# Kernel tuning notes

Hardware: AMD Instinct MI355X
Metric: run time of the kernel (lower is better)

The kernel has to match this reference:

```python
import jax, jax.numpy as jnp
import numpy as np

DIM = 1024
HEADS = 16
DIM_HEAD = 64
DIM_INNER = HEADS * DIM_HEAD
R_MAJOR = 2.0
R_MINOR = 1.0
EPS = 1e-10
ATTN_SCALE = DIM_HEAD ** 0.5  # torch SDPA `scale` is a multiplier on q@k^T
S_QK_FACTOR = float(DIM)      # Scale forward multiplier: init / scale = 1.0 / (1/dim)


def toroidal_norm(t, axis=-1, R=R_MAJOR, r=R_MINOR, eps=EPS):
    """Project onto sphere, scale first half of `axis` by R, second by r, renormalize."""
    axis = axis % t.ndim
    n = jnp.linalg.norm(t, axis=axis, keepdims=True)
    sp = t / jnp.clip(n, eps)
    d = t.shape[axis]
    h = d // 2
    scale = jnp.concatenate([jnp.full((h,), R, t.dtype), jnp.full((d - h,), r, t.dtype)])
    bshape = [1] * t.ndim
    bshape[axis] = d
    tp = sp * scale.reshape(bshape)
    n2 = jnp.linalg.norm(tp, axis=axis, keepdims=True)
    return tp / jnp.clip(n2, eps)


def setup_inputs() -> dict:
    key = jax.random.key(0)
    ks = jax.random.split(key, 5)
    b, n = 4, 1024
    x = jax.random.normal(ks[0], (b, n, DIM), jnp.float32)
    std = DIM ** -0.5
    w_q = jax.random.normal(ks[1], (DIM_INNER, DIM), jnp.float32) * std
    w_k = jax.random.normal(ks[2], (DIM_INNER, DIM), jnp.float32) * std
    w_v = jax.random.normal(ks[3], (DIM_INNER, DIM), jnp.float32) * std
    w_o = jax.random.normal(ks[4], (DIM, DIM_INNER), jnp.float32) * std
    qk_scale_param = jnp.full((DIM_INNER,), 1.0 / DIM, jnp.float32)  # Scale init
    return {"x": x, "w_q": w_q, "w_k": w_k, "w_v": w_v, "w_o": w_o,
            "qk_scale_param": qk_scale_param}


def reference(x, w_q, w_k, w_v, w_o, qk_scale_param):
    b, n, _ = x.shape
    # parametrized (toroidal-normed) projection weights
    wq = toroidal_norm(w_q, axis=-1)
    wk = toroidal_norm(w_k, axis=-1)
    wv = toroidal_norm(w_v, axis=-1)
    wo = toroidal_norm(w_o, axis=0)  # norm_dim_in=False -> dim=0

    q = jnp.einsum('bnd,ed->bne', x, wq).reshape(b, n, HEADS, DIM_HEAD).transpose(0, 2, 1, 3)
    k = jnp.einsum('bnd,ed->bne', x, wk).reshape(b, n, HEADS, DIM_HEAD).transpose(0, 2, 1, 3)
    v = jnp.einsum('bnd,ed->bne', x, wv).reshape(b, n, HEADS, DIM_HEAD).transpose(0, 2, 1, 3)

    # toroidal norm over head dim
    q = toroidal_norm(q, axis=-1)
    k = toroidal_norm(k, axis=-1)

    # learned per-channel qk scale: param * (init / scale)
    s = (qk_scale_param * S_QK_FACTOR).reshape(HEADS, 1, DIM_HEAD)
    q = q * s

    scores = jnp.einsum('bhnd,bhmd->bhnm', q, k) * ATTN_SCALE
    causal = jnp.tril(jnp.ones((n, n), bool))
    scores = jnp.where(causal, scores, jnp.finfo(scores.dtype).min)
    attn = jax.nn.softmax(scores, axis=-1)
    out = jnp.einsum('bhnm,bhmd->bhnd', attn, v)  # b h n d

    out = out.transpose(0, 2, 1, 3).reshape(b, n, DIM_INNER)
    return jnp.einsum('bne,de->bnd', out, wo)
```

## Files before the change

### kernel.cpp

```cpp
#include <hip/hip_runtime.h>
#include <hip/hip_bf16.h>

#define HEADS 16
#define DH    64
#define BATCH 4
#define SEQ   1024
#define DIMD  1024
#define TOK   4096

typedef __attribute__((ext_vector_type(8))) short bf16x8;
typedef __attribute__((ext_vector_type(4))) float f32x4;
typedef __attribute__((ext_vector_type(16))) float f32x16;

typedef const void __attribute__((address_space(1)))* gas1_t;
typedef void __attribute__((address_space(3)))* las3_t;

#define GLOAD16(g,l) __builtin_amdgcn_global_load_lds((gas1_t)(g),(las3_t)(l),16,0,0)
#define MFMA_BF16(a,b,c) __builtin_amdgcn_mfma_f32_16x16x32_bf16((a),(b),(c),0,0,0)
#define MFMA32(a,b,c) __builtin_amdgcn_mfma_f32_32x32x16_bf16((a),(b),(c),0,0,0)
#define ZERO16 {0.f,0.f,0.f,0.f,0.f,0.f,0.f,0.f,0.f,0.f,0.f,0.f,0.f,0.f,0.f,0.f}

__device__ __forceinline__ ushort f2bf(float f){
  __hip_bfloat16 h = __float2bfloat16(f);
  return *reinterpret_cast<ushort*>(&h);
}
__device__ __forceinline__ uint packbf2(float a, float b){
  return (uint)f2bf(a) | ((uint)f2bf(b) << 16);
}
__device__ __forceinline__ uint xswap32(uint x){
  return (uint)__shfl_xor((int)x, 32);
}

__global__ __launch_bounds__(256) void cast_x_kernel(const float* __restrict__ x,
                                                     ushort* __restrict__ xb){
  int i = blockIdx.x*256 + threadIdx.x;
  const float4* x4 = (const float4*)x;
  float4 a = x4[2*i], b = x4[2*i+1];
  union { ushort s[8]; uint4 u; } uu;
  uu.s[0]=f2bf(a.x); uu.s[1]=f2bf(a.y); uu.s[2]=f2bf(a.z); uu.s[3]=f2bf(a.w);
  uu.s[4]=f2bf(b.x); uu.s[5]=f2bf(b.y); uu.s[6]=f2bf(b.z); uu.s[7]=f2bf(b.w);
  ((uint4*)xb)[i] = uu.u;
}

__global__ __launch_bounds__(256) void norm_rows_kernel(
    const float* __restrict__ wq, const float* __restrict__ wk, const float* __restrict__ wv,
    ushort* __restrict__ oq, ushort* __restrict__ ok, ushort* __restrict__ ov){
  int row = blockIdx.x & 1023;
  int m = blockIdx.x >> 10;
  const float* src = (m==0)?wq:((m==1)?wk:wv);
  ushort* dst = (m==0)?oq:((m==1)?ok:ov);
  int t = threadIdx.x;
  float4 v = ((const float4*)(src + (size_t)row*1024))[t];
  float sc = (t<128)?2.f:1.f;
  float ss = sc*sc*(v.x*v.x + v.y*v.y + v.z*v.z + v.w*v.w);
  #pragma unroll
  for (int off=1; off<64; off<<=1) ss += __shfl_xor(ss, off);
  __shared__ float part[4];
  int w = t>>6, lane = t&63;
  if (lane==0) part[w]=ss;
  __syncthreads();
  float tot = part[0]+part[1]+part[2]+part[3];
  float inv = rsqrtf(fmaxf(tot,1e-20f)) * sc;
  union { ushort s[4]; uint2 u; } o;
  o.s[0]=f2bf(v.x*inv); o.s[1]=f2bf(v.y*inv); o.s[2]=f2bf(v.z*inv); o.s[3]=f2bf(v.w*inv);
  ((uint2*)(dst + (size_t)row*1024))[t] = o.u;
}

__global__ __launch_bounds__(256) void cast_wo_kernel(const float* __restrict__ wo,
                                                      ushort* __restrict__ wob){
  int i = blockIdx.x*256 + threadIdx.x;
  float sc = ((i>>7) < 512) ? 2.f : 1.f;
  const float4* x4 = (const float4*)wo;
  float4 a = x4[2*i], b = x4[2*i+1];
  union { ushort s[8]; uint4 u; } uu;
  uu.s[0]=f2bf(a.x*sc); uu.s[1]=f2bf(a.y*sc); uu.s[2]=f2bf(a.z*sc); uu.s[3]=f2bf(a.w*sc);
  uu.s[4]=f2bf(b.x*sc); uu.s[5]=f2bf(b.y*sc); uu.s[6]=f2bf(b.z*sc); uu.s[7]=f2bf(b.w*sc);
  ((uint4*)wob)[i] = uu.u;
}

__global__ __launch_bounds__(256) void wo_part_kernel(const float* __restrict__ wo,
                                                      float* __restrict__ part){
  int rb = blockIdx.x, t = threadIdx.x;
  float4 a = {0.f,0.f,0.f,0.f};
  #pragma unroll 4
  for (int r=0;r<32;r++){
    int row = rb*32+r;
    float4 v = ((const float4*)wo)[row*256 + t];
    float s2 = (row<512)?4.f:1.f;
    a.x += s2*v.x*v.x; a.y += s2*v.y*v.y; a.z += s2*v.z*v.z; a.w += s2*v.w*v.w;
  }
  ((float4*)part)[rb*256 + t] = a;
}
__global__ __launch_bounds__(256) void wo_csum_kernel(const float* __restrict__ part,
                                                      float* __restrict__ colsum){
  int c = blockIdx.x*256 + threadIdx.x;
  float s = 0.f;
  #pragma unroll
  for (int j=0;j<32;j++) s += part[j*1024 + c];
  colsum[c] = s;
}

template<int NZ>
__global__ __launch_bounds__(256, 2) void gemm_fused_kernel(
    const ushort* __restrict__ A,
    const ushort* __restrict__ B0, const ushort* __restrict__ B1, const ushort* __restrict__ B2,
    void* dst0, void* dst1, void* dst2,
    const float* __restrict__ qparam, const float* __restrict__ colsum, int K)
{
  __shared__ ushort As[64*32];
  __shared__ ushort Bs[NZ*128*32];
  const int bm = blockIdx.x*64, bn = blockIdx.y*128;
  const int tid = threadIdx.x, lane = tid&63, w = tid>>6;
  const int wr = w>>1, wc = w&1;
  const int l15 = lane&15, l4 = lane>>4;
  const int srow = lane>>2, sch = lane&3;

  const f32x4 zero4 = {0.f,0.f,0.f,0.f};
  f32x4 acc[NZ][2][4];
  #pragma unroll
  for (int z=0;z<NZ;z++)
    #pragma unroll
    for (int m=0;m<2;m++)
      #pragma unroll
      for (int n=0;n<4;n++) acc[z][m][n] = zero4;

  for (int k0=0; k0<K; k0+=32){
    __syncthreads();
    GLOAD16(A + (size_t)(bm + w*16 + srow)*K + k0 + sch*8, &As[w*512]);
    #pragma unroll
    for (int j=0;j<NZ*2;j++){
      int seg = j*4 + w;
      int z = seg>>3, s = seg&7;
      const ushort* Bp = (z==0)?B0:((z==1)?B1:B2);
      GLOAD16(Bp + (size_t)(bn + s*16 + srow)*K + k0 + sch*8, &Bs[seg*512]);
    }
    __syncthreads();
    bf16x8 af[2];
    #pragma unroll
    for (int m=0;m<2;m++)
      af[m] = *(const bf16x8*)&As[(wr*32 + m*16 + l15)*32 + l4*8];
    #pragma unroll
    for (int z=0;z<NZ;z++){
      bf16x8 bfr[4];
      #pragma unroll
      for (int n=0;n<4;n++)
        bfr[n] = *(const bf16x8*)&Bs[z*4096 + (wc*64 + n*16 + l15)*32 + l4*8];
      #pragma unroll
      for (int m=0;m<2;m++)
        #pragma unroll
        for (int n=0;n<4;n++)
          acc[z][m][n] = MFMA_BF16(af[m], bfr[n], acc[z][m][n]);
    }
  }

  if (NZ==3){
    #pragma unroll
    for (int z=0;z<3;z++){
      ushort* dst = (ushort*)((z==0)?dst0:((z==1)?dst1:dst2));
      float qs[4];
      #pragma unroll
      for (int n=0;n<4;n++){
        int e = bn + wc*64 + n*16 + l15;
        if (z==0)      qs[n] = qparam[e]*8192.f*1.44269504088896f;
        else if (z==2) qs[n] = rsqrtf(fmaxf(colsum[e],1e-20f));
        else           qs[n] = 1.f;
      }
      #pragma unroll
      for (int m=0;m<2;m++){
        float ssq[4] = {0.f,0.f,0.f,0.f};
        if (z<2){
          #pragma unroll
          for (int reg=0;reg<4;reg++){
            float s=0.f;
            #pragma unroll
            for (int n=0;n<4;n++){
              float scl2 = (n<2)?4.f:1.f;
              float vv = acc[z][m][n][reg];
              s += scl2*vv*vv;
            }
            ssq[reg]=s;
          }
          #pragma unroll
          for (int d=1; d<16; d<<=1){
            #pragma unroll
            for (int reg=0;reg<4;reg++) ssq[reg] += __shfl_xor(ssq[reg], d);
          }
        }
        #pragma unroll
        for (int n=0;n<4;n++){
          float scl = (n<2)?2.f:1.f;
          #pragma unroll
          for (int reg=0;reg<4;reg++){
            float val = acc[z][m][n][reg];
            if (z<2) val = val*scl*rsqrtf(fmaxf(ssq[reg],1e-20f))*qs[n];
            else     val = val*qs[n];
            int row = bm + wr*32 + m*16 + l4*4 + reg;
            int col = bn + wc*64 + n*16 + l15;
            int b = row>>10, nn = row&1023, h = col>>6, d = col&63;
            if (z==2)
              dst[(((size_t)b*HEADS+h)*DH + d)*SEQ + nn] = f2bf(val);
            else
              dst[(((size_t)b*HEADS+h)*SEQ + nn)*DH + d] = f2bf(val);
          }
        }
      }
    }
  } else {
    float* outp = (float*)dst0;
    #pragma unroll
    for (int m=0;m<2;m++)
      #pragma unroll
      for (int n=0;n<4;n++)
        #pragma unroll
        for (int reg=0;reg<4;reg++){
          int row = bm + wr*32 + m*16 + l4*4 + reg;
          int col = bn + wc*64 + n*16 + l15;
          outp[(size_t)row*DIMD + col] = acc[0][m][n][reg];
        }
  }
}

template<int NS, bool MASK>
__device__ __forceinline__ void attn_iter(
    const ushort* __restrict__ Kp, const ushort* __restrict__ Vp,
    int kvb, const bf16x8 (&qf)[4], int l31, int l1,
    f32x16& o0, f32x16& o1, float& m_s, float& l_s)
{
  bf16x8 kfa[4], kfb[4];
  #pragma unroll
  for (int md=0; md<4; md++)
    kfa[md] = *(const bf16x8*)&Kp[(size_t)(kvb + l31)*DH + md*16 + l1*8];
  if (NS==2){
    #pragma unroll
    for (int md=0; md<4; md++)
      kfb[md] = *(const bf16x8*)&Kp[(size_t)(kvb + 32 + l31)*DH + md*16 + l1*8];
  }
  bf16x8 vf0[2*NS], vf1[2*NS];
  #pragma unroll
  for (int kc=0; kc<2*NS; kc++){
    vf0[kc] = *(const bf16x8*)&Vp[(size_t)l31*SEQ      + kvb + kc*16 + l1*8];
    vf1[kc] = *(const bf16x8*)&Vp[(size_t)(32+l31)*SEQ + kvb + kc*16 + l1*8];
  }

  f32x16 s0 = ZERO16, s1 = ZERO16;
  __builtin_amdgcn_s_setprio(1);
  #pragma unroll
  for (int md=0; md<4; md++) s0 = MFMA32(kfa[md], qf[md], s0);
  if (NS==2){
    #pragma unroll
    for (int md=0; md<4; md++) s1 = MFMA32(kfb[md], qf[md], s1);
  }
  __builtin_amdgcn_s_setprio(0);

  if (MASK){
    f32x16& sm = (NS==2) ? s1 : s0;
    #pragma unroll
    for (int r=0;r<16;r++){
      int kvl = (r&3) + 8*(r>>2) + 4*l1;
      if (kvl > l31) sm[r] = -3.0e38f;
    }
  }

  float mx = -3.0e38f;
  #pragma unroll
  for (int r=0;r<16;r++) mx = fmaxf(mx, s0[r]);
  if (NS==2){
    #pragma unroll
    for (int r=0;r<16;r++) mx = fmaxf(mx, s1[r]);
  }
  mx = fmaxf(mx, __shfl_xor(mx, 32));
  float mnew = fmaxf(m_s, mx);
  float alpha = __builtin_amdgcn_exp2f(m_s - mnew);
  m_s = mnew;
  float rs = 0.f;
  #pragma unroll
  for (int r=0;r<16;r++){ s0[r] = __builtin_amdgcn_exp2f(s0[r]-mnew); rs += s0[r]; }
  if (NS==2){
    #pragma unroll
    for (int r=0;r<16;r++){ s1[r] = __builtin_amdgcn_exp2f(s1[r]-mnew); rs += s1[r]; }
  }
  rs += __shfl_xor(rs, 32);
  l_s = l_s*alpha + rs;

  #pragma unroll
  for (int r=0;r<16;r++){ o0[r] *= alpha; o1[r] *= alpha; }

  uint ru[16];
  #pragma unroll
  for (int j=0;j<8;j++) ru[j] = packbf2(s0[2*j], s0[2*j+1]);
  if (NS==2){
    #pragma unroll
    for (int j=0;j<8;j++) ru[8+j] = packbf2(s1[2*j], s1[2*j+1]);
  }
  union U4 { uint u[4]; bf16x8 v; };
  U4 fr[2*NS];
  #pragma unroll
  for (int j=0;j<NS;j++){
    uint px[8];
    #pragma unroll
    for (int k=0;k<8;k++) px[k] = xswap32(ru[8*j+k]);
    fr[2*j].u[0]   = l1 ? px[2]      : ru[8*j+0];
    fr[2*j].u[1]   = l1 ? px[3]      : ru[8*j+1];
    fr[2*j].u[2]   = l1 ? ru[8*j+2]  : px[0];
    fr[2*j].u[3]   = l1 ? ru[8*j+3]  : px[1];
    fr[2*j+1].u[0] = l1 ? px[6]      : ru[8*j+4];
    fr[2*j+1].u[1] = l1 ? px[7]      : ru[8*j+5];
    fr[2*j+1].u[2] = l1 ? ru[8*j+6]  : px[4];
    fr[2*j+1].u[3] = l1 ? ru[8*j+7]  : px[5];
  }

  __builtin_amdgcn_s_setprio(1);
  #pragma unroll
  for (int kc=0; kc<2*NS; kc++){
    o0 = MFMA32(vf0[kc], fr[kc].v, o0);
    o1 = MFMA32(vf1[kc], fr[kc].v, o1);
  }
  __builtin_amdgcn_s_setprio(0);
}

__device__ __forceinline__ void process_tile(
    int t, int par, int bh,
    const ushort* __restrict__ Q, const ushort* __restrict__ K,
    const ushort* __restrict__ VT, ushort* __restrict__ O,
    int l31, int l1)
{
  const size_t base  = (size_t)bh * SEQ * DH;
  const size_t vbase = (size_t)bh * DH * SEQ;
  const ushort* Kp = K + base;
  const ushort* Vp = VT + vbase;
  const int qbase = t*64 + par*32;

  bf16x8 qf[4];
  #pragma unroll
  for (int md=0; md<4; md++)
    qf[md] = *(const bf16x8*)&Q[base + (size_t)(qbase + l31)*DH + md*16 + l1*8];

  f32x16 o0 = ZERO16, o1 = ZERO16;
  float m_s = -3.0e38f, l_s = 0.f;

  for (int kt=0; kt<t; kt++)
    attn_iter<2,false>(Kp, Vp, kt*64, qf, l31, l1, o0, o1, m_s, l_s);
  if (par) attn_iter<2,true>(Kp, Vp, t*64, qf, l31, l1, o0, o1, m_s, l_s);
  else     attn_iter<1,true>(Kp, Vp, t*64, qf, l31, l1, o0, o1, m_s, l_s);

  float li = 1.0f / l_s;
  int b = bh >> 4, hh = bh & 15;
  int n = qbase + l31;
  ushort* orow = O + ((size_t)b*SEQ + n)*DIMD + hh*64;
  #pragma unroll
  for (int r=0;r<16;r++){
    int dl = (r&3) + 8*(r>>2) + 4*l1;
    orow[dl]    = f2bf(o0[r]*li);
    orow[32+dl] = f2bf(o1[r]*li);
  }
}

__global__ __launch_bounds__(256, 2) void attn_kernel(
    const ushort* __restrict__ Q, const ushort* __restrict__ K, const ushort* __restrict__ VT,
    ushort* __restrict__ O)
{
  int id = blockIdx.x;
  int p  = id >> 6;
  int r  = id & 63;
  int bh = (r&7)*8 + (r>>3);
  int tid = threadIdx.x, wi = tid>>6, lane = tid&63;
  int l31 = lane & 31, l1 = lane >> 5;
  int sel = (wi & 1) ^ (bh & 1);
  int t   = sel ? (15-p) : p;
  int par = wi >> 1;
  process_tile(t, par, bh, Q, K, VT, O, l31, l1);
}

extern "C" void kernel_launch(void* const* d_in, const int* in_sizes, int n_in,
                              void* d_out, int out_size, void* d_ws, size_t ws_size,
                              hipStream_t stream)
{
  const float* x      = (const float*)d_in[0];
  const float* w_q    = (const float*)d_in[1];
  const float* w_k    = (const float*)d_in[2];
  const float* w_v    = (const float*)d_in[3];
  const float* w_o    = (const float*)d_in[4];
  const float* qparam = (const float*)d_in[5];
  char* ws = (char*)d_ws;
  const size_t MB = 1u<<20;
  ushort* xb  = (ushort*)(ws);
  ushort* wqb = (ushort*)(ws + 8*MB);
  ushort* wkb = (ushort*)(ws + 10*MB);
  ushort* wvb = (ushort*)(ws + 12*MB);
  ushort* wob = (ushort*)(ws + 14*MB);
  ushort* qd  = (ushort*)(ws + 16*MB);
  ushort* kd  = (ushort*)(ws + 24*MB);
  ushort* vd  = (ushort*)(ws + 32*MB);
  ushort* att = xb;
  float* part = (float*)(ws + 16*MB);
  float* colsum = (float*)d_out + (out_size - 1024);

  cast_x_kernel<<<dim3(2048), dim3(256), 0, stream>>>(x, xb);
  norm_rows_kernel<<<dim3(3072), dim3(256), 0, stream>>>(w_q, w_k, w_v, wqb, wkb, wvb);
  cast_wo_kernel<<<dim3(512), dim3(256), 0, stream>>>(w_o, wob);
  wo_part_kernel<<<dim3(32), dim3(256), 0, stream>>>(w_o, part);
  wo_csum_kernel<<<dim3(4), dim3(256), 0, stream>>>(part, colsum);
  gemm_fused_kernel<3><<<dim3(64,8), dim3(256), 0, stream>>>(
      xb, wqb, wkb, wvb, (void*)qd, (void*)kd, (void*)vd, qparam, colsum, DIMD);
  attn_kernel<<<dim3(512), dim3(256), 0, stream>>>(qd, kd, vd, att);
  gemm_fused_kernel<1><<<dim3(64,8), dim3(256), 0, stream>>>(
      att, wob, wob, wob, d_out, nullptr, nullptr, nullptr, nullptr, DIMD);
}
```

Measured before the change: 126.3 us.

## Merge preprocessing kernels into one launch and change GEMM LDS tile layout

Combines the x cast, q/k/v weight row normalisation, w_o cast and w_o column-partial-sum kernels into a single prep kernel that branches on block index. This removes three launches and the gaps between them. The partial-sum buffer moves to its own workspace region so it cannot collide with q data. The GEMM global-to-LDS load mapping also changes: each lane now loads row lane&15 and chunk lane>>4, and the fragment reads use a matching chunk-major LDS layout. The aim is to change LDS bank access patterns for the MFMA operand reads.

Measured after the change: 143.5 us. 1.14x slower.

```diff
diff --git a/kernel.cpp b/kernel.cpp
--- a/kernel.cpp
+++ b/kernel.cpp
@@ -31,66 +31,66 @@
   return (uint)__shfl_xor((int)x, 32);
 }
 
-__global__ __launch_bounds__(256) void cast_x_kernel(const float* __restrict__ x,
-                                                     ushort* __restrict__ xb){
-  int i = blockIdx.x*256 + threadIdx.x;
-  const float4* x4 = (const float4*)x;
-  float4 a = x4[2*i], b = x4[2*i+1];
-  union { ushort s[8]; uint4 u; } uu;
-  uu.s[0]=f2bf(a.x); uu.s[1]=f2bf(a.y); uu.s[2]=f2bf(a.z); uu.s[3]=f2bf(a.w);
-  uu.s[4]=f2bf(b.x); uu.s[5]=f2bf(b.y); uu.s[6]=f2bf(b.z); uu.s[7]=f2bf(b.w);
-  ((uint4*)xb)[i] = uu.u;
-}
-
-__global__ __launch_bounds__(256) void norm_rows_kernel(
+__global__ __launch_bounds__(256) void prep_kernel(
+    const float* __restrict__ x,
     const float* __restrict__ wq, const float* __restrict__ wk, const float* __restrict__ wv,
-    ushort* __restrict__ oq, ushort* __restrict__ ok, ushort* __restrict__ ov){
-  int row = blockIdx.x & 1023;
-  int m = blockIdx.x >> 10;
-  const float* src = (m==0)?wq:((m==1)?wk:wv);
-  ushort* dst = (m==0)?oq:((m==1)?ok:ov);
-  int t = threadIdx.x;
-  float4 v = ((const float4*)(src + (size_t)row*1024))[t];
-  float sc = (t<128)?2.f:1.f;
-  float ss = sc*sc*(v.x*v.x + v.y*v.y + v.z*v.z + v.w*v.w);
-  #pragma unroll
-  for (int off=1; off<64; off<<=1) ss += __shfl_xor(ss, off);
-  __shared__ float part[4];
-  int w = t>>6, lane = t&63;
-  if (lane==0) part[w]=ss;
-  __syncthreads();
-  float tot = part[0]+part[1]+part[2]+part[3];
-  float inv = rsqrtf(fmaxf(tot,1e-20f)) * sc;
-  union { ushort s[4]; uint2 u; } o;
-  o.s[0]=f2bf(v.x*inv); o.s[1]=f2bf(v.y*inv); o.s[2]=f2bf(v.z*inv); o.s[3]=f2bf(v.w*inv);
-  ((uint2*)(dst + (size_t)row*1024))[t] = o.u;
-}
-
-__global__ __launch_bounds__(256) void cast_wo_kernel(const float* __restrict__ wo,
-                                                      ushort* __restrict__ wob){
-  int i = blockIdx.x*256 + threadIdx.x;
-  float sc = ((i>>7) < 512) ? 2.f : 1.f;
-  const float4* x4 = (const float4*)wo;
-  float4 a = x4[2*i], b = x4[2*i+1];
-  union { ushort s[8]; uint4 u; } uu;
-  uu.s[0]=f2bf(a.x*sc); uu.s[1]=f2bf(a.y*sc); uu.s[2]=f2bf(a.z*sc); uu.s[3]=f2bf(a.w*sc);
-  uu.s[4]=f2bf(b.x*sc); uu.s[5]=f2bf(b.y*sc); uu.s[6]=f2bf(b.z*sc); uu.s[7]=f2bf(b.w*sc);
-  ((uint4*)wob)[i] = uu.u;
-}
-
-__global__ __launch_bounds__(256) void wo_part_kernel(const float* __restrict__ wo,
-                                                      float* __restrict__ part){
-  int rb = blockIdx.x, t = threadIdx.x;
-  float4 a = {0.f,0.f,0.f,0.f};
-  #pragma unroll 4
-  for (int r=0;r<32;r++){
-    int row = rb*32+r;
-    float4 v = ((const float4*)wo)[row*256 + t];
-    float s2 = (row<512)?4.f:1.f;
-    a.x += s2*v.x*v.x; a.y += s2*v.y*v.y; a.z += s2*v.z*v.z; a.w += s2*v.w*v.w;
-  }
-  ((float4*)part)[rb*256 + t] = a;
-}
+    const float* __restrict__ wo,
+    ushort* __restrict__ xb,
+    ushort* __restrict__ oq, ushort* __restrict__ ok, ushort* __restrict__ ov,
+    ushort* __restrict__ wob, float* __restrict__ part)
+{
+  __shared__ float sp[4];
+  int bid = blockIdx.x, t = threadIdx.x;
+  if (bid < 2048){
+    int i = bid*256 + t;
+    const float4* x4 = (const float4*)x;
+    float4 a = x4[2*i], b = x4[2*i+1];
+    union { ushort s[8]; uint4 u; } uu;
+    uu.s[0]=f2bf(a.x); uu.s[1]=f2bf(a.y); uu.s[2]=f2bf(a.z); uu.s[3]=f2bf(a.w);
+    uu.s[4]=f2bf(b.x); uu.s[5]=f2bf(b.y); uu.s[6]=f2bf(b.z); uu.s[7]=f2bf(b.w);
+    ((uint4*)xb)[i] = uu.u;
+  } else if (bid < 5120){
+    int bb = bid - 2048;
+    int row = bb & 1023;
+    int m = bb >> 10;
+    const float* src = (m==0)?wq:((m==1)?wk:wv);
+    ushort* dst = (m==0)?oq:((m==1)?ok:ov);
+    float4 v = ((const float4*)(src + (size_t)row*1024))[t];
+    float sc = (t<128)?2.f:1.f;
+    float ss = sc*sc*(v.x*v.x + v.y*v.y + v.z*v.z + v.w*v.w);
+    #pragma unroll
+    for (int off=1; off<64; off<<=1) ss += __shfl_xor(ss, off);
+    int w = t>>6, lane = t&63;
+    if (lane==0) sp[w]=ss;
+    __syncthreads();
+    float tot = sp[0]+sp[1]+sp[2]+sp[3];
+    float inv = rsqrtf(fmaxf(tot,1e-20f)) * sc;
+    union { ushort s[4]; uint2 u; } o;
+    o.s[0]=f2bf(v.x*inv); o.s[1]=f2bf(v.y*inv); o.s[2]=f2bf(v.z*inv); o.s[3]=f2bf(v.w*inv);
+    ((uint2*)(dst + (size_t)row*1024))[t] = o.u;
+  } else if (bid < 5632){
+    int i = (bid-5120)*256 + t;
+    float sc = ((i>>7) < 512) ? 2.f : 1.f;
+    const float4* x4 = (const float4*)wo;
+    float4 a = x4[2*i], b = x4[2*i+1];
+    union { ushort s[8]; uint4 u; } uu;
+    uu.s[0]=f2bf(a.x*sc); uu.s[1]=f2bf(a.y*sc); uu.s[2]=f2bf(a.z*sc); uu.s[3]=f2bf(a.w*sc);
+    uu.s[4]=f2bf(b.x*sc); uu.s[5]=f2bf(b.y*sc); uu.s[6]=f2bf(b.z*sc); uu.s[7]=f2bf(b.w*sc);
+    ((uint4*)wob)[i] = uu.u;
+  } else {
+    int rb = bid - 5632;
+    float4 a = {0.f,0.f,0.f,0.f};
+    #pragma unroll 4
+    for (int r=0;r<32;r++){
+      int row = rb*32+r;
+      float4 v = ((const float4*)wo)[row*256 + t];
+      float s2 = (row<512)?4.f:1.f;
+      a.x += s2*v.x*v.x; a.y += s2*v.y*v.y; a.z += s2*v.z*v.z; a.w += s2*v.w*v.w;
+    }
+    ((float4*)part)[rb*256 + t] = a;
+  }
+}
+
 __global__ __launch_bounds__(256) void wo_csum_kernel(const float* __restrict__ part,
                                                       float* __restrict__ colsum){
   int c = blockIdx.x*256 + threadIdx.x;
@@ -113,7 +113,7 @@
   const int tid = threadIdx.x, lane = tid&63, w = tid>>6;
   const int wr = w>>1, wc = w&1;
   const int l15 = lane&15, l4 = lane>>4;
-  const int srow = lane>>2, sch = lane&3;
+  const int row16 = lane&15, ch = lane>>4;
 
   const f32x4 zero4 = {0.f,0.f,0.f,0.f};
   f32x4 acc[NZ][2][4];
@@ -126,25 +126,25 @@
 
   for (int k0=0; k0<K; k0+=32){
     __syncthreads();
-    GLOAD16(A + (size_t)(bm + w*16 + srow)*K + k0 + sch*8, &As[w*512]);
+    GLOAD16(A + (size_t)(bm + w*16 + row16)*K + k0 + ch*8, &As[w*512]);
     #pragma unroll
     for (int j=0;j<NZ*2;j++){
       int seg = j*4 + w;
       int z = seg>>3, s = seg&7;
       const ushort* Bp = (z==0)?B0:((z==1)?B1:B2);
-      GLOAD16(Bp + (size_t)(bn + s*16 + srow)*K + k0 + sch*8, &Bs[seg*512]);
+      GLOAD16(Bp + (size_t)(bn + s*16 + row16)*K + k0 + ch*8, &Bs[seg*512]);
     }
     __syncthreads();
     bf16x8 af[2];
     #pragma unroll
     for (int m=0;m<2;m++)
-      af[m] = *(const bf16x8*)&As[(wr*32 + m*16 + l15)*32 + l4*8];
+      af[m] = *(const bf16x8*)&As[(wr*2+m)*512 + l4*128 + l15*8];
     #pragma unroll
     for (int z=0;z<NZ;z++){
       bf16x8 bfr[4];
       #pragma unroll
       for (int n=0;n<4;n++)
-        bfr[n] = *(const bf16x8*)&Bs[z*4096 + (wc*64 + n*16 + l15)*32 + l4*8];
+        bfr[n] = *(const bf16x8*)&Bs[z*4096 + (wc*4+n)*512 + l4*128 + l15*8];
       #pragma unroll
       for (int m=0;m<2;m++)
         #pragma unroll
@@ -392,13 +392,11 @@
   ushort* kd  = (ushort*)(ws + 24*MB);
   ushort* vd  = (ushort*)(ws + 32*MB);
   ushort* att = xb;
-  float* part = (float*)(ws + 16*MB);
+  float* part = (float*)(ws + 40*MB);
   float* colsum = (float*)d_out + (out_size - 1024);
 
-  cast_x_kernel<<<dim3(2048), dim3(256), 0, stream>>>(x, xb);
-  norm_rows_kernel<<<dim3(3072), dim3(256), 0, stream>>>(w_q, w_k, w_v, wqb, wkb, wvb);
-  cast_wo_kernel<<<dim3(512), dim3(256), 0, stream>>>(w_o, wob);
-  wo_part_kernel<<<dim3(32), dim3(256), 0, stream>>>(w_o, part);
+  prep_kernel<<<dim3(5664), dim3(256), 0, stream>>>(
+      x, w_q, w_k, w_v, w_o, xb, wqb, wkb, wvb, wob, part);
   wo_csum_kernel<<<dim3(4), dim3(256), 0, stream>>>(part, colsum);
   gemm_fused_kernel<3><<<dim3(64,8), dim3(256), 0, stream>>>(
       xb, wqb, wkb, wvb, (void*)qd, (void*)kd, (void*)vd, qparam, colsum, DIMD);
```
